# Performance work log

Measured on AMD Instinct MI355X. Metric: run time of the kernel, lower is better.

## Reference

```python
import jax, jax.numpy as jnp
import numpy as np

B, N, OUTERDIM, DIM, N_CLASSES = 2, 6000, 1024, 512, 2
HEADS, DIM_HEAD, INNER = 8, 64, 512
LANDMARKS, PINV_ITERS, KPAD = 256, 6, 16  # residual conv kernel 33 -> pad 16
SCALE = DIM_HEAD ** -0.5


def layer_norm(x, g, b, eps=1e-5):
    mu = x.mean(-1, keepdims=True)
    var = jnp.var(x, axis=-1, keepdims=True)
    return (x - mu) * jax.lax.rsqrt(var + eps) * g + b


def moore_penrose_pinv(x, iters=PINV_ITERS):
    # x: [b, h, m, m]
    abs_x = jnp.abs(x)
    col = abs_x.sum(-1)
    row = abs_x.sum(-2)
    z = jnp.swapaxes(x, -1, -2) / (jnp.max(col) * jnp.max(row))
    I = jnp.eye(x.shape[-1], dtype=x.dtype)
    for _ in range(iters):
        xz = x @ z
        z = 0.25 * z @ (13 * I - xz @ (15 * I - xz @ (7 * I - xz)))
    return z


def nystrom_attention(x, w_qkv, w_out, b_out, conv_w):
    b, n, _ = x.shape
    pad = (-n) % LANDMARKS
    xp = jnp.pad(x, ((0, 0), (pad, 0), (0, 0)))  # pad at FRONT, as in lucidrains impl
    npad = n + pad
    qkv = xp @ w_qkv.T  # [b, npad, 3*inner]
    q, k, v = [t.reshape(b, npad, HEADS, DIM_HEAD).transpose(0, 2, 1, 3)
               for t in jnp.split(qkv, 3, axis=-1)]
    q = q * SCALE
    l = npad // LANDMARKS  # tokens per landmark
    q_l = q.reshape(b, HEADS, LANDMARKS, l, DIM_HEAD).sum(3) / l
    k_l = k.reshape(b, HEADS, LANDMARKS, l, DIM_HEAD).sum(3) / l
    attn1 = jax.nn.softmax(jnp.einsum('bhid,bhjd->bhij', q, k_l), axis=-1)   # [b,h,npad,m]
    attn2 = jax.nn.softmax(jnp.einsum('bhid,bhjd->bhij', q_l, k_l), axis=-1)  # [b,h,m,m]
    attn3 = jax.nn.softmax(jnp.einsum('bhid,bhjd->bhij', q_l, k), axis=-1)    # [b,h,m,npad]
    out = (attn1 @ moore_penrose_pinv(attn2)) @ (attn3 @ v)  # [b,h,npad,d]
    # depthwise residual conv over sequence dim (per head), kernel (33,1)
    out = out + jax.lax.conv_general_dilated(
        v, conv_w, window_strides=(1, 1), padding=((KPAD, KPAD), (0, 0)),
        dimension_numbers=('NCHW', 'OIHW', 'NCHW'), feature_group_count=HEADS)
    out = out.transpose(0, 2, 1, 3).reshape(b, npad, INNER)
    out = out @ w_out.T + b_out
    return out[:, -n:]


def setup_inputs() -> dict:
    key = jax.random.key(0)
    ks = jax.random.split(key, 12)
    w = lambda k, shape: 0.02 * jax.random.normal(k, shape, dtype=jnp.float32)
    inp = {
        'data': jax.random.normal(ks[0], (B, N, OUTERDIM), dtype=jnp.float32),
        'w1': w(ks[1], (DIM, OUTERDIM)), 'b1': jnp.zeros((DIM,), jnp.float32),
        'cls_token': jax.random.normal(ks[2], (1, 1, DIM), dtype=jnp.float32),
        'ln1_g': jnp.ones((DIM,), jnp.float32), 'ln1_b': jnp.zeros((DIM,), jnp.float32),
        'qkv1_w': w(ks[3], (3 * INNER, DIM)),
        'out1_w': w(ks[4], (DIM, INNER)), 'out1_b': jnp.zeros((DIM,), jnp.float32),
        'conv1_w': w(ks[5], (HEADS, 1, 33, 1)),
        'ln2_g': jnp.ones((DIM,), jnp.float32), 'ln2_b': jnp.zeros((DIM,), jnp.float32),
        'qkv2_w': w(ks[6], (3 * INNER, DIM)),
        'out2_w': w(ks[7], (DIM, INNER)), 'out2_b': jnp.zeros((DIM,), jnp.float32),
        'conv2_w': w(ks[8], (HEADS, 1, 33, 1)),
        'lnf_g': jnp.ones((DIM,), jnp.float32), 'lnf_b': jnp.zeros((DIM,), jnp.float32),
        'w2': w(ks[9], (N_CLASSES, DIM)), 'b2': jnp.zeros((N_CLASSES,), jnp.float32),
    }
    return inp


def reference(data, w1, b1, cls_token, ln1_g, ln1_b, qkv1_w, out1_w, out1_b, conv1_w,
              ln2_g, ln2_b, qkv2_w, out2_w, out2_b, conv2_w, lnf_g, lnf_b, w2, b2):
    h = jax.nn.relu(data @ w1.T + b1)  # [B, N, DIM]
    H = h.shape[1]
    side = int(np.ceil(np.sqrt(H)))
    add = side * side - H
    h = jnp.concatenate([h, h[:, :add]], axis=1)  # square padding: 6084
    cls = jnp.broadcast_to(cls_token, (h.shape[0], 1, h.shape[2]))
    h = jnp.concatenate([cls, h], axis=1)  # +CLS: 6085
    h = h + nystrom_attention(layer_norm(h, ln1_g, ln1_b), qkv1_w, out1_w, out1_b, conv1_w)
    h = h + nystrom_attention(layer_norm(h, ln2_g, ln2_b), qkv2_w, out2_w, out2_b, conv2_w)
    h = layer_norm(h, lnf_g, lnf_b)[:, 0]
    logits = h @ w2.T + b2
    return logits
```

## Files before the change

### kernel.cpp

```cpp
#include <hip/hip_runtime.h>
#include <cstdint>
#include <cstddef>

namespace {

constexpr int DIMC  = 512;
constexpr int SEQ   = 6085;
constexpr int NPAD  = 6144;
constexpr int PADF  = 59;
constexpr int LMK   = 256;
constexpr int BHN   = 16;
constexpr int KSPL  = 16;
constexpr int MPADR = 6016;

typedef __attribute__((ext_vector_type(8))) short bf8_t;
typedef __attribute__((ext_vector_type(4))) float f4_t;

#define SWZB(r, cu) (((((r) << 6) + ((cu) << 1))) ^ (((r) & 7) << 4))

#define GLDS16(gp, lp) __builtin_amdgcn_global_load_lds( \
    (const __attribute__((address_space(1))) void*)(gp), \
    (__attribute__((address_space(3))) void*)(lp), 16, 0, 0)

__device__ __forceinline__ ushort f2bf(float f) {
    union { float f; uint32_t u; } c{f};
    uint32_t u = c.u;
    return (ushort)((u + 0x7FFFu + ((u >> 16) & 1u)) >> 16);
}
__device__ __forceinline__ float bf2f(ushort u) {
    union { uint32_t u; float f; } c{(uint32_t)u << 16};
    return c.f;
}

__device__ __forceinline__ float waveSum(float v) {
#pragma unroll
    for (int o = 32; o > 0; o >>= 1) v += __shfl_xor(v, o, 64);
    return v;
}
__device__ __forceinline__ float waveMax(float v) {
#pragma unroll
    for (int o = 32; o > 0; o >>= 1) v = fmaxf(v, __shfl_xor(v, o, 64));
    return v;
}
__device__ __forceinline__ float blockSum256(float v, float* sm) {
    v = waveSum(v);
    __syncthreads();
    if ((threadIdx.x & 63) == 0) sm[threadIdx.x >> 6] = v;
    __syncthreads();
    return sm[0] + sm[1] + sm[2] + sm[3];
}
__device__ __forceinline__ float blockMax256(float v, float* sm) {
    v = waveMax(v);
    __syncthreads();
    if ((threadIdx.x & 63) == 0) sm[threadIdx.x >> 6] = v;
    __syncthreads();
    return fmaxf(fmaxf(sm[0], sm[1]), fmaxf(sm[2], sm[3]));
}

template<int EPI>
__global__ __launch_bounds__(256)
void gemm_bt(const ushort* __restrict__ A, const ushort* __restrict__ B,
             void* __restrict__ Cv, int M, int N, int K,
             int lda, int ldb, int ldc,
             long long sA, long long sB, long long sC,
             const float* __restrict__ bias, int relu,
             ushort* __restrict__ qp, ushort* __restrict__ kp, ushort* __restrict__ vp)
{
    __shared__ __align__(16) char As_s[128 * 128];
    __shared__ __align__(16) char Bs_s[128 * 128];
    const int z = blockIdx.z;
    const ushort* Ab = A + (size_t)z * sA;
    const ushort* Bb = B + (size_t)z * sB;
    const int row0 = blockIdx.y * 128, col0 = blockIdx.x * 128;
    const int tid = threadIdx.x, wid = tid >> 6, lane = tid & 63;
    const int wr = wid >> 1, wc = wid & 1, lr = lane & 15, kg = lane >> 4;
    const int srow = lane >> 3, sq = lane & 7;
    f4_t acc[4][4] = {};
    for (int k0 = 0; k0 < K; k0 += 64) {
        __syncthreads();
#pragma unroll
        for (int i = 0; i < 4; ++i) {
            int r = wid * 32 + i * 8 + srow;
            int qs = sq ^ (r & 7);
            GLDS16(Ab + (size_t)(row0 + r) * lda + k0 + qs * 8,
                   As_s + (wid * 32 + i * 8) * 128);
        }
#pragma unroll
        for (int i = 0; i < 4; ++i) {
            int r = wid * 32 + i * 8 + srow;
            int qs = sq ^ (r & 7);
            GLDS16(Bb + (size_t)(col0 + r) * ldb + k0 + qs * 8,
                   Bs_s + (wid * 32 + i * 8) * 128);
        }
        asm volatile("s_waitcnt vmcnt(0)" ::: "memory");
        __syncthreads();
#pragma unroll
        for (int ks = 0; ks < 2; ++ks) {
            bf8_t af[4], bg[4];
#pragma unroll
            for (int mr = 0; mr < 4; ++mr) {
                int r = wr * 64 + mr * 16 + lr;
                af[mr] = *(const bf8_t*)(As_s + r * 128 + ((((ks << 2) | kg) ^ (r & 7)) << 4));
            }
#pragma unroll
            for (int nr = 0; nr < 4; ++nr) {
                int r = wc * 64 + nr * 16 + lr;
                bg[nr] = *(const bf8_t*)(Bs_s + r * 128 + ((((ks << 2) | kg) ^ (r & 7)) << 4));
            }
#pragma unroll
            for (int mr = 0; mr < 4; ++mr)
#pragma unroll
                for (int nr = 0; nr < 4; ++nr)
                    acc[mr][nr] = __builtin_amdgcn_mfma_f32_16x16x32_bf16(af[mr], bg[nr], acc[mr][nr], 0, 0, 0);
        }
    }
#pragma unroll
    for (int mr = 0; mr < 4; ++mr) {
#pragma unroll
        for (int nr = 0; nr < 4; ++nr) {
#pragma unroll
            for (int r = 0; r < 4; ++r) {
                int gm = row0 + wr * 64 + mr * 16 + kg * 4 + r;
                int gn = col0 + wc * 64 + nr * 16 + lr;
                if (gm >= M || gn >= N) continue;
                float val = acc[mr][nr][r];
                if (EPI == 0) {
                    if (bias) val += bias[gn];
                    if (relu) val = fmaxf(val, 0.f);
                    ((float*)Cv)[(size_t)z * sC + (size_t)gm * ldc + gn] = val;
                } else if (EPI == 1) {
                    ((ushort*)Cv)[(size_t)z * sC + (size_t)gm * ldc + gn] = f2bf(val);
                } else {
                    int b = (gm >= NPAD) ? 1 : 0;
                    int i = gm - b * NPAD;
                    int which = gn >> 9, hh = (gn >> 6) & 7, d = gn & 63;
                    size_t dst = ((size_t)(b * 8 + hh) * NPAD + i) * 64 + d;
                    if (which == 0)      qp[dst] = f2bf(val * 0.125f);
                    else if (which == 1) kp[dst] = f2bf(val);
                    else                 vp[dst] = f2bf(val);
                }
            }
        }
    }
}

__global__ __launch_bounds__(256)
void attn1_fused(const ushort* __restrict__ q, const ushort* __restrict__ kl,
                 const ushort* __restrict__ Wt, ushort* __restrict__ ot)
{
    __shared__ __align__(16) char P_s[128 * 512];
    const int mt = blockIdx.x;
    const int bh = blockIdx.y;
    const int b = bh >> 3, hh = bh & 7;
    const int tid = threadIdx.x, wid = tid >> 6, lane = tid & 63;
    const int lr = lane & 15, kg = lane >> 4;
    const int row0 = mt * 128;
    const ushort* qb  = q  + (size_t)bh * NPAD * 64;
    const ushort* klb = kl + (size_t)bh * LMK * 64;
    const ushort* Wtb = Wt + (size_t)bh * 128 * 256;

    f4_t acc[2][16];
#pragma unroll
    for (int mf = 0; mf < 2; ++mf)
#pragma unroll
        for (int nf = 0; nf < 16; ++nf) acc[mf][nf] = (f4_t){0.f, 0.f, 0.f, 0.f};
#pragma unroll
    for (int ks = 0; ks < 2; ++ks) {
        bf8_t af[2];
#pragma unroll
        for (int mf = 0; mf < 2; ++mf)
            af[mf] = *(const bf8_t*)&qb[(size_t)(row0 + wid * 32 + mf * 16 + lr) * 64 + ks * 32 + kg * 8];
#pragma unroll
        for (int nf = 0; nf < 16; ++nf) {
            bf8_t bg = *(const bf8_t*)&klb[(size_t)(nf * 16 + lr) * 64 + ks * 32 + kg * 8];
            acc[0][nf] = __builtin_amdgcn_mfma_f32_16x16x32_bf16(af[0], bg, acc[0][nf], 0, 0, 0);
            acc[1][nf] = __builtin_amdgcn_mfma_f32_16x16x32_bf16(af[1], bg, acc[1][nf], 0, 0, 0);
        }
    }
    float inv_s[2][4];
#pragma unroll
    for (int mf = 0; mf < 2; ++mf) {
        float mx[4] = {-1e30f, -1e30f, -1e30f, -1e30f};
#pragma unroll
        for (int nf = 0; nf < 16; ++nf)
#pragma unroll
            for (int r = 0; r < 4; ++r) mx[r] = fmaxf(mx[r], acc[mf][nf][r]);
#pragma unroll
        for (int r = 0; r < 4; ++r) {
            mx[r] = fmaxf(mx[r], __shfl_xor(mx[r], 1, 64));
            mx[r] = fmaxf(mx[r], __shfl_xor(mx[r], 2, 64));
            mx[r] = fmaxf(mx[r], __shfl_xor(mx[r], 4, 64));
            mx[r] = fmaxf(mx[r], __shfl_xor(mx[r], 8, 64));
        }
        float sum[4] = {0.f, 0.f, 0.f, 0.f};
        const int rowb = wid * 32 + mf * 16 + kg * 4;
        const int cc2 = (lr & 7) * 2;
        const int chi = lr >> 3;
#pragma unroll
        for (int nf = 0; nf < 16; ++nf) {
#pragma unroll
            for (int r = 0; r < 4; ++r) {
                float e = expf(acc[mf][nf][r] - mx[r]);
                sum[r] += e;
                int row = rowb + r;
                int chunk = (2 * nf + chi) ^ (row & 7);
                *(ushort*)(P_s + row * 512 + chunk * 16 + cc2) = f2bf(e);
            }
        }
#pragma unroll
        for (int r = 0; r < 4; ++r) {
            sum[r] += __shfl_xor(sum[r], 1, 64);
            sum[r] += __shfl_xor(sum[r], 2, 64);
            sum[r] += __shfl_xor(sum[r], 4, 64);
            sum[r] += __shfl_xor(sum[r], 8, 64);
            inv_s[mf][r] = 1.f / sum[r];
        }
    }
    f4_t acc2[2][4] = {};
#pragma unroll
    for (int kt = 0; kt < 8; ++kt) {
        bf8_t af2[2];
#pragma unroll
        for (int mf = 0; mf < 2; ++mf) {
            int row = wid * 32 + mf * 16 + lr;
            int chunk = (kt * 4 + kg) ^ (row & 7);
            af2[mf] = *(const bf8_t*)(P_s + row * 512 + chunk * 16);
        }
#pragma unroll
        for (int nf = 0; nf < 4; ++nf) {
            bf8_t bg = *(const bf8_t*)&Wtb[(size_t)(nf * 16 + lr) * 256 + kt * 32 + kg * 8];
            acc2[0][nf] = __builtin_amdgcn_mfma_f32_16x16x32_bf16(af2[0], bg, acc2[0][nf], 0, 0, 0);
            acc2[1][nf] = __builtin_amdgcn_mfma_f32_16x16x32_bf16(af2[1], bg, acc2[1][nf], 0, 0, 0);
        }
    }
#pragma unroll
    for (int mf = 0; mf < 2; ++mf)
#pragma unroll
        for (int nf = 0; nf < 4; ++nf)
#pragma unroll
            for (int r = 0; r < 4; ++r) {
                int gm = row0 + wid * 32 + mf * 16 + kg * 4 + r;
                int gn = nf * 16 + lr;
                ot[((size_t)(b * NPAD + gm)) * DIMC + hh * 64 + gn] =
                    f2bf(acc2[mf][nf][r] * inv_s[mf][r]);
            }
}

__global__ __launch_bounds__(256)
void gemm_ns(const ushort* __restrict__ A, const ushort* __restrict__ B,
             ushort* __restrict__ C, ushort* __restrict__ C2, ushort* __restrict__ CT,
             float alpha, float c2d, int K, int N,
             long long sA, long long sB, long long sC, long long sCT)
{
    __shared__ __align__(16) char As_s[64 * 64];
    __shared__ __align__(16) char Bs_s[64 * 64];
    const int z = blockIdx.z;
    const int row0 = blockIdx.y * 64, col0 = blockIdx.x * 64;
    const int tid = threadIdx.x;
    const int wid = tid >> 6, lane = tid & 63;
    const int lr = lane & 15, kg = lane >> 4;
    const ushort* Ab = A + (size_t)z * sA;
    const ushort* Bb = B + (size_t)z * sB;
    f4_t acc[4] = {};
    const int am = tid >> 2, ac8 = (tid & 3) * 8;
    for (int k0 = 0; k0 < K; k0 += 32) {
        *(bf8_t*)(As_s + SWZB(am, ac8)) = *(const bf8_t*)&Ab[(size_t)(row0 + am) * K + k0 + ac8];
#pragma unroll
        for (int p = 0; p < 8; ++p) {
            int kk = p * 4 + (tid >> 6), n = tid & 63;
            *(ushort*)(Bs_s + SWZB(n, kk)) = Bb[(size_t)(k0 + kk) * N + col0 + n];
        }
        __syncthreads();
        bf8_t af = *(const bf8_t*)(As_s + SWZB(wid * 16 + lr, kg * 8));
#pragma unroll
        for (int j = 0; j < 4; ++j) {
            bf8_t bg = *(const bf8_t*)(Bs_s + SWZB(j * 16 + lr, kg * 8));
            acc[j] = __builtin_amdgcn_mfma_f32_16x16x32_bf16(af, bg, acc[j], 0, 0, 0);
        }
        __syncthreads();
    }
#pragma unroll
    for (int j = 0; j < 4; ++j) {
#pragma unroll
        for (int r = 0; r < 4; ++r) {
            int gm = row0 + wid * 16 + kg * 4 + r;
            int gn = col0 + j * 16 + lr;
            float val = alpha * acc[j][r];
            if (C)  C[(size_t)z * sC + (size_t)gm * N + gn] = f2bf(val);
            if (C2) C2[(size_t)z * sC + (size_t)gm * N + gn] = f2bf(((gm == gn) ? c2d : 0.f) - val);
            if (CT) CT[(size_t)z * sCT + (size_t)gn * LMK + gm] = f2bf(val);
        }
    }
}

__global__ __launch_bounds__(256)
void pv_splitk(const ushort* __restrict__ S, const ushort* __restrict__ v,
               float* __restrict__ o2p)
{
    __shared__ __align__(16) char As_s[128 * 64];
    __shared__ __align__(16) char Bs_s[64 * 64];
    const int split = blockIdx.x, mt = blockIdx.y, bh = blockIdx.z;
    const int tid = threadIdx.x;
    const int wid = tid >> 6, lane = tid & 63;
    const int lr = lane & 15, kg = lane >> 4;
    const ushort* Sb = S + (size_t)bh * LMK * NPAD + (size_t)(mt * 128) * NPAD;
    const ushort* vb = v + (size_t)bh * NPAD * 64;
    const int ks0 = split * (NPAD / KSPL);
    f4_t acc[2][4] = {};
    for (int k0 = ks0; k0 < ks0 + NPAD / KSPL; k0 += 32) {
#pragma unroll
        for (int p = 0; p < 2; ++p) {
            int idx = p * 256 + tid;
            int m = idx >> 2, kc = (idx & 3) * 8;
            *(bf8_t*)(As_s + SWZB(m, kc)) = *(const bf8_t*)&Sb[(size_t)m * NPAD + k0 + kc];
        }
#pragma unroll
        for (int p = 0; p < 8; ++p) {
            int kk = p * 4 + (tid >> 6), n = tid & 63;
            *(ushort*)(Bs_s + SWZB(n, kk)) = vb[(size_t)(k0 + kk) * 64 + n];
        }
        __syncthreads();
        bf8_t af[2], bg[4];
#pragma unroll
        for (int i = 0; i < 2; ++i)
            af[i] = *(const bf8_t*)(As_s + SWZB(wid * 32 + i * 16 + lr, kg * 8));
#pragma unroll
        for (int j = 0; j < 4; ++j)
            bg[j] = *(const bf8_t*)(Bs_s + SWZB(j * 16 + lr, kg * 8));
#pragma unroll
        for (int i = 0; i < 2; ++i)
#pragma unroll
            for (int j = 0; j < 4; ++j)
                acc[i][j] = __builtin_amdgcn_mfma_f32_16x16x32_bf16(af[i], bg[j], acc[i][j], 0, 0, 0);
        __syncthreads();
    }
#pragma unroll
    for (int i = 0; i < 2; ++i)
#pragma unroll
        for (int j = 0; j < 4; ++j)
#pragma unroll
            for (int r = 0; r < 4; ++r) {
                int gm = mt * 128 + wid * 32 + i * 16 + kg * 4 + r;
                int gn = j * 16 + lr;
                o2p[((size_t)(split * BHN + bh) * LMK + gm) * 64 + gn] = acc[i][j][r];
            }
}

__global__ void reduce_o2(const float* __restrict__ o2p, ushort* __restrict__ o2) {
    int idx = blockIdx.x * 256 + threadIdx.x;
    int bh = idx >> 14, e = idx & 16383;
    float s = 0.f;
#pragma unroll
    for (int sp = 0; sp < KSPL; ++sp)
        s += o2p[((size_t)(sp * BHN + bh) << 14) + e];
    o2[idx] = f2bf(s);
}

__global__ void cvt_bf16(const float* __restrict__ in, ushort* __restrict__ out, int n8) {
    int i = blockIdx.x * 256 + threadIdx.x;
    if (i >= n8) return;
    float4 a = ((const float4*)in)[i * 2], b = ((const float4*)in)[i * 2 + 1];
    ushort4 lo = { f2bf(a.x), f2bf(a.y), f2bf(a.z), f2bf(a.w) };
    ushort4 hi = { f2bf(b.x), f2bf(b.y), f2bf(b.z), f2bf(b.w) };
    ((ushort4*)out)[i * 2] = lo;
    ((ushort4*)out)[i * 2 + 1] = hi;
}

__global__ void extend_h(float* __restrict__ h, const float* __restrict__ cls) {
    int b = blockIdx.y, bx = blockIdx.x;
    float* hb = h + (size_t)b * SEQ * DIMC;
    for (int c = threadIdx.x; c < DIMC; c += 256) {
        if (bx == 0) hb[c] = cls[c];
        else hb[(size_t)(6000 + bx) * DIMC + c] = hb[(size_t)bx * DIMC + c];
    }
}

__global__ void zero_xp_pad(ushort* __restrict__ xp) {
    int e = blockIdx.x * 256 + threadIdx.x;
    int b = e / (PADF * DIMC);
    int rest = e - b * (PADF * DIMC);
    xp[(size_t)b * NPAD * DIMC + rest] = 0;
}

__global__ __launch_bounds__(128)
void ln_to_xp(const float* __restrict__ h, const float* __restrict__ g,
              const float* __restrict__ bb, ushort* __restrict__ xp)
{
    __shared__ float sm[2];
    int r = blockIdx.x;
    int b = r / SEQ, i = r - b * SEQ;
    int t = threadIdx.x;
    const float4* row = (const float4*)(h + (size_t)r * DIMC);
    float4 x = row[t];
    float s  = x.x + x.y + x.z + x.w;
    float sq = x.x * x.x + x.y * x.y + x.z * x.z + x.w * x.w;
    s = waveSum(s);
    sq = waveSum(sq);
    int w = t >> 6;
    if ((t & 63) == 0) sm[w] = s;
    __syncthreads();
    float S = sm[0] + sm[1];
    __syncthreads();
    if ((t & 63) == 0) sm[w] = sq;
    __syncthreads();
    float SQ = sm[0] + sm[1];
    float mu = S * (1.f / DIMC);
    float var = SQ * (1.f / DIMC) - mu * mu;
    float rs = rsqrtf(var + 1e-5f);
    float4 gg = ((const float4*)g)[t];
    float4 bv = ((const float4*)bb)[t];
    ushort4 o;
    o.x = f2bf((x.x - mu) * rs * gg.x + bv.x);
    o.y = f2bf((x.y - mu) * rs * gg.y + bv.y);
    o.z = f2bf((x.z - mu) * rs * gg.z + bv.z);
    o.w = f2bf((x.w - mu) * rs * gg.w + bv.w);
    ((ushort4*)(xp + ((size_t)b * NPAD + PADF + i) * DIMC))[t] = o;
}

__global__ void landmark_mean(const ushort* __restrict__ in, ushort* __restrict__ out) {
    int m = blockIdx.x, bh = blockIdx.y, d = threadIdx.x;
    const ushort* p = in + ((size_t)bh * NPAD + (size_t)m * (NPAD / LMK)) * 64 + d;
    float s = 0.f;
#pragma unroll
    for (int j = 0; j < NPAD / LMK; ++j) s += bf2f(p[(size_t)j * 64]);
    out[((size_t)bh * LMK + m) * 64 + d] = f2bf(s * (1.f / (NPAD / LMK)));
}

__global__ __launch_bounds__(256)
void softmax_bf_wide(ushort* __restrict__ S) {
    __shared__ float sm[4];
    ushort* p = S + (size_t)blockIdx.x * NPAD;
    int t = threadIdx.x;
    float v[24];
    float mx = -1e30f;
#pragma unroll
    for (int j = 0; j < 24; ++j) { v[j] = bf2f(p[j * 256 + t]); mx = fmaxf(mx, v[j]); }
    float bm = blockMax256(mx, sm);
    float s = 0.f;
#pragma unroll
    for (int j = 0; j < 24; ++j) { v[j] = expf(v[j] - bm); s += v[j]; }
    float bs = blockSum256(s, sm);
    float inv = 1.f / bs;
#pragma unroll
    for (int j = 0; j < 24; ++j) p[j * 256 + t] = f2bf(v[j] * inv);
}

__global__ __launch_bounds__(256)
void softmax_bf256(ushort* __restrict__ S) {
    __shared__ float sm[4];
    ushort* p = S + (size_t)blockIdx.x * 256;
    int t = threadIdx.x;
    float v = bf2f(p[t]);
    float bm = blockMax256(v, sm);
    float e = expf(v - bm);
    float bs = blockSum256(e, sm);
    p[t] = f2bf(e / bs);
}

__global__ __launch_bounds__(256)
void colsum_max(const ushort* __restrict__ X, float* __restrict__ scal) {
    __shared__ float sm[4];
    int bh = blockIdx.x, t = threadIdx.x;
    const ushort* Xb = X + ((size_t)bh << 16);
    float s = 0.f;
#pragma unroll 8
    for (int i = 0; i < 256; ++i) s += bf2f(Xb[(size_t)i * 256 + t]);
    float m = blockMax256(s, sm);
    if (t == 0) atomicMax((unsigned int*)scal, __float_as_uint(m));
}

__global__ void init_z(const ushort* __restrict__ X, const float* __restrict__ scal,
                       ushort* __restrict__ Z) {
    size_t e = (size_t)blockIdx.x * 256 + threadIdx.x;
    int c = (int)(e & 255);
    int r = (int)((e >> 8) & 255);
    size_t bh = e >> 16;
    float inv = 1.f / scal[0];
    Z[e] = f2bf(bf2f(X[(bh << 16) + (size_t)c * 256 + r]) * inv);
}

__global__ __launch_bounds__(256)
void conv_add(const ushort* __restrict__ v, const float* __restrict__ cw,
              ushort* __restrict__ ot)
{
    __shared__ float w[33];
    __shared__ ushort vt[96][64];
    int bh = blockIdx.y;
    int b = bh >> 3, hh = bh & 7;
    int i0 = blockIdx.x * 64;
    int t = threadIdx.x;
    if (t < 33) w[t] = cw[hh * 33 + t];
    const ushort* vb = v + (size_t)bh * NPAD * 64;
    int d = t & 63;
    for (int rr = t >> 6; rr < 96; rr += 4) {
        int j = i0 - 16 + rr;
        vt[rr][d] = (j >= 0 && j < NPAD) ? vb[(size_t)j * 64 + d] : (ushort)0;
    }
    __syncthreads();
    for (int ii = t >> 6; ii < 64; ii += 4) {
        float acc = 0.f;
#pragma unroll
        for (int kk = 0; kk < 33; ++kk) acc += w[kk] * bf2f(vt[ii + kk][d]);
        size_t off = ((size_t)(b * NPAD + i0 + ii)) * DIMC + hh * 64 + d;
        ot[off] = f2bf(bf2f(ot[off]) + acc);
    }
}

__global__ void residual_add(float* __restrict__ h, const float* __restrict__ y) {
    size_t e = (size_t)blockIdx.x * 256 + threadIdx.x;
    int c = (int)(e & 511);
    size_t ri = e >> 9;
    int i = (int)(ri % SEQ);
    int b = (int)(ri / SEQ);
    h[e] += y[((size_t)b * NPAD + PADF + i) * DIMC + c];
}

__global__ __launch_bounds__(256)
void final_head(const float* __restrict__ h, const float* __restrict__ g,
                const float* __restrict__ bb, const float* __restrict__ w2,
                const float* __restrict__ b2, float* __restrict__ out)
{
    __shared__ float row[DIMC];
    __shared__ float sm[4];
    int b = blockIdx.x;
    int t = threadIdx.x;
    const float* x = h + (size_t)b * SEQ * DIMC;
    float v0 = x[t], v1 = x[t + 256];
    float S = blockSum256(v0 + v1, sm);
    float SQ = blockSum256(v0 * v0 + v1 * v1, sm);
    float mu = S * (1.f / DIMC);
    float rs = rsqrtf(SQ * (1.f / DIMC) - mu * mu + 1e-5f);
    row[t] = (v0 - mu) * rs * g[t] + bb[t];
    row[t + 256] = (v1 - mu) * rs * g[t + 256] + bb[t + 256];
    __syncthreads();
    if (t < 64) {
        float a0 = 0.f, a1 = 0.f;
        for (int idx = t; idx < DIMC; idx += 64) {
            a0 += row[idx] * w2[idx];
            a1 += row[idx] * w2[DIMC + idx];
        }
        a0 = waveSum(a0);
        a1 = waveSum(a1);
        if (t == 0) {
            out[b * 2 + 0] = a0 + b2[0];
            out[b * 2 + 1] = a1 + b2[1];
        }
    }
}

void bt(int epi, const ushort* A, const ushort* B, void* C, int M, int N, int K,
        int lda, int ldb, int ldc, long long sA, long long sB, long long sC, int batch,
        const float* bias, int relu, ushort* qp, ushort* kp, ushort* vp, hipStream_t s)
{
    dim3 g((N + 127) / 128, (M + 127) / 128, batch), blk(256);
    switch (epi) {
    case 0: gemm_bt<0><<<g, blk, 0, s>>>(A, B, C, M, N, K, lda, ldb, ldc, sA, sB, sC, bias, relu, qp, kp, vp); break;
    case 1: gemm_bt<1><<<g, blk, 0, s>>>(A, B, C, M, N, K, lda, ldb, ldc, sA, sB, sC, bias, relu, qp, kp, vp); break;
    default: gemm_bt<2><<<g, blk, 0, s>>>(A, B, C, M, N, K, lda, ldb, ldc, sA, sB, sC, bias, relu, qp, kp, vp); break;
    }
}

void ns(const ushort* A, const ushort* B, ushort* C, ushort* C2, ushort* CT,
        float alpha, float c2d, int M, int N, int K,
        long long sA, long long sB, long long sC, long long sCT, hipStream_t s)
{
    dim3 g(N / 64, M / 64, BHN), blk(256);
    gemm_ns<<<g, blk, 0, s>>>(A, B, C, C2, CT, alpha, c2d, K, N, sA, sB, sC, sCT);
}

struct WS {
    float *h, *scal, *o2p, *y;
    ushort *xp, *q, *k, *v, *ql, *kl;
    ushort *datab, *w1b, *qkvwb1, *qkvwb2, *outwb1, *outwb2;
    ushort *X, *Z0, *Z1, *XZ, *TA, *TB, *TC;
    ushort *o2b, *Wt, *S, *ot;
};

void nystrom_layer(float* h, const float* lng, const float* lnb,
                   const ushort* qkvwb, const ushort* outwb, const float* outb,
                   const float* convw, const WS& w, hipStream_t s)
{
    const long long SM = (long long)LMK * LMK;
    zero_xp_pad<<<(2 * PADF * DIMC) / 256, 256, 0, s>>>(w.xp);
    ln_to_xp<<<2 * SEQ, 128, 0, s>>>(h, lng, lnb, w.xp);
    bt(2, w.xp, qkvwb, nullptr, 2 * NPAD, 3 * DIMC, DIMC, DIMC, DIMC, 0,
       0, 0, 0, 1, nullptr, 0, w.q, w.k, w.v, s);
    landmark_mean<<<dim3(LMK, BHN), 64, 0, s>>>(w.q, w.ql);
    landmark_mean<<<dim3(LMK, BHN), 64, 0, s>>>(w.k, w.kl);
    bt(1, w.ql, w.kl, w.X, LMK, LMK, 64, 64, 64, LMK,
       (long long)LMK * 64, (long long)LMK * 64, SM, BHN, nullptr, 0, nullptr, nullptr, nullptr, s);
    softmax_bf256<<<BHN * LMK, 256, 0, s>>>(w.X);
    hipMemsetAsync(w.scal, 0, 8, s);
    colsum_max<<<BHN, 256, 0, s>>>(w.X, w.scal);
    init_z<<<(BHN * LMK * LMK) / 256, 256, 0, s>>>(w.X, w.scal, w.Z0);
    ushort* Zc = w.Z0;
    ushort* Zn = w.Z1;
    for (int it = 0; it < 6; ++it) {
        ns(w.X, Zc, w.XZ, w.TA, nullptr, 1.f, 7.f, LMK, LMK, LMK, SM, SM, SM, 0, s);
        ns(w.XZ, w.TA, w.TB, w.TC, nullptr, 1.f, 15.f, LMK, LMK, LMK, SM, SM, SM, 0, s);
        ns(w.XZ, w.TC, w.TB, w.TA, nullptr, 1.f, 13.f, LMK, LMK, LMK, SM, SM, SM, 0, s);
        ns(Zc, w.TA, Zn, nullptr, nullptr, 0.25f, 0.f, LMK, LMK, LMK, SM, SM, SM, 0, s);
        ushort* t = Zc; Zc = Zn; Zn = t;
    }
    bt(1, w.ql, w.k, w.S, LMK, NPAD, 64, 64, 64, NPAD,
       (long long)LMK * 64, (long long)NPAD * 64, (long long)LMK * NPAD, BHN,
       nullptr, 0, nullptr, nullptr, nullptr, s);
    softmax_bf_wide<<<BHN * LMK, 256, 0, s>>>(w.S);
    pv_splitk<<<dim3(KSPL, 2, BHN), 256, 0, s>>>(w.S, w.v, w.o2p);
    reduce_o2<<<BHN * LMK * 64 / 256, 256, 0, s>>>(w.o2p, w.o2b);
    ns(Zc, w.o2b, nullptr, nullptr, w.Wt, 1.f, 0.f, LMK, 64, LMK,
       SM, (long long)LMK * 64, 0, 128 * 256, s);
    attn1_fused<<<dim3(NPAD / 128, BHN), 256, 0, s>>>(w.q, w.kl, w.Wt, w.ot);
    conv_add<<<dim3(NPAD / 64, BHN), 256, 0, s>>>(w.v, convw, w.ot);
    bt(0, w.ot, outwb, w.y, 2 * NPAD, DIMC, DIMC, DIMC, DIMC, DIMC,
       0, 0, 0, 1, outb, 0, nullptr, nullptr, nullptr, s);
    residual_add<<<(2 * SEQ * DIMC) / 256, 256, 0, s>>>(h, w.y);
}

}

extern "C" void kernel_launch(void* const* d_in, const int* in_sizes, int n_in,
                              void* d_out, int out_size, void* d_ws, size_t ws_size,
                              hipStream_t stream)
{
    (void)in_sizes; (void)n_in; (void)out_size;
    const float* data  = (const float*)d_in[0];
    const float* w1    = (const float*)d_in[1];
    const float* b1    = (const float*)d_in[2];
    const float* cls   = (const float*)d_in[3];
    const float* ln1g  = (const float*)d_in[4];
    const float* ln1b  = (const float*)d_in[5];
    const float* qkv1w = (const float*)d_in[6];
    const float* out1w = (const float*)d_in[7];
    const float* out1b = (const float*)d_in[8];
    const float* conv1 = (const float*)d_in[9];
    const float* ln2g  = (const float*)d_in[10];
    const float* ln2b  = (const float*)d_in[11];
    const float* qkv2w = (const float*)d_in[12];
    const float* out2w = (const float*)d_in[13];
    const float* out2b = (const float*)d_in[14];
    const float* conv2 = (const float*)d_in[15];
    const float* lnfg  = (const float*)d_in[16];
    const float* lnfb  = (const float*)d_in[17];
    const float* w2    = (const float*)d_in[18];
    const float* b2    = (const float*)d_in[19];
    float* out = (float*)d_out;

    if (ws_size < 209473792ull) return;
    char* p = (char*)d_ws;
    auto alloc = [&](size_t bytes) { char* r = p; p += (bytes + 255) & ~(size_t)255; return r; };
    WS w;
    w.h     = (float*)alloc((size_t)2 * SEQ * DIMC * 4);
    w.xp    = (ushort*)alloc((size_t)2 * NPAD * DIMC * 2);
    w.q     = (ushort*)alloc((size_t)BHN * NPAD * 64 * 2);
    w.k     = (ushort*)alloc((size_t)BHN * NPAD * 64 * 2);
    w.v     = (ushort*)alloc((size_t)BHN * NPAD * 64 * 2);
    w.ql    = (ushort*)alloc((size_t)BHN * LMK * 64 * 2);
    w.kl    = (ushort*)alloc((size_t)BHN * LMK * 64 * 2);
    w.scal  = (float*)alloc(256);
    w.datab = (ushort*)alloc((size_t)2 * MPADR * 1024 * 2);
    w.w1b   = (ushort*)alloc((size_t)512 * 1024 * 2);
    w.qkvwb1= (ushort*)alloc((size_t)1536 * 512 * 2);
    w.qkvwb2= (ushort*)alloc((size_t)1536 * 512 * 2);
    w.outwb1= (ushort*)alloc((size_t)512 * 512 * 2);
    w.outwb2= (ushort*)alloc((size_t)512 * 512 * 2);
    w.X     = (ushort*)alloc((size_t)BHN * LMK * LMK * 2);
    w.Z0    = (ushort*)alloc((size_t)BHN * LMK * LMK * 2);
    w.Z1    = (ushort*)alloc((size_t)BHN * LMK * LMK * 2);
    w.XZ    = (ushort*)alloc((size_t)BHN * LMK * LMK * 2);
    w.TA    = (ushort*)alloc((size_t)BHN * LMK * LMK * 2);
    w.TB    = (ushort*)alloc((size_t)BHN * LMK * LMK * 2);
    w.TC    = (ushort*)alloc((size_t)BHN * LMK * LMK * 2);
    w.o2p   = (float*)alloc((size_t)KSPL * BHN * LMK * 64 * 4);
    w.o2b   = (ushort*)alloc((size_t)BHN * LMK * 64 * 2);
    w.Wt    = (ushort*)alloc((size_t)BHN * 128 * 256 * 2);
    w.S     = (ushort*)alloc((size_t)BHN * LMK * NPAD * 2);
    w.y     = (float*)w.S;
    w.ot    = w.k;

    for (int b = 0; b < 2; ++b)
        cvt_bf16<<<3000, 256, 0, stream>>>(data + (size_t)b * 6000 * 1024,
                                           w.datab + (size_t)b * MPADR * 1024, 768000);
    cvt_bf16<<<256, 256, 0, stream>>>(w1, w.w1b, 65536);
    cvt_bf16<<<384, 256, 0, stream>>>(qkv1w, w.qkvwb1, 98304);
    cvt_bf16<<<384, 256, 0, stream>>>(qkv2w, w.qkvwb2, 98304);
    cvt_bf16<<<128, 256, 0, stream>>>(out1w, w.outwb1, 32768);
    cvt_bf16<<<128, 256, 0, stream>>>(out2w, w.outwb2, 32768);

    bt(0, w.datab, w.w1b, w.h + DIMC, 6000, DIMC, 1024, 1024, 1024, DIMC,
       (long long)MPADR * 1024, 0, (long long)SEQ * DIMC, 2, b1, 1,
       nullptr, nullptr, nullptr, stream);
    extend_h<<<dim3(85, 2), 256, 0, stream>>>(w.h, cls);

    nystrom_layer(w.h, ln1g, ln1b, w.qkvwb1, w.outwb1, out1b, conv1, w, stream);
    nystrom_layer(w.h, ln2g, ln2b, w.qkvwb2, w.outwb2, out2b, conv2, w, stream);

    final_head<<<2, 256, 0, stream>>>(w.h, lnfg, lnfb, w2, b2, out);
}
```

Before: 1.019 ms.

## Remap GEMM blocks across XCDs, halve attn1 tile rows, use fast exp

Block indices in the generic GEMM are remapped so that consecutive tiles land on the same XCD, which should improve L2 reuse on the multi-die part. attn1_fused now handles 64 rows per block with one 16-row fragment per wave, halving the accumulator registers and shared memory to raise occupancy and double the grid. Softmax kernels switch expf to __expf, trading a little accuracy for cheaper exponentials.

```diff
diff --git a/kernel.cpp b/kernel.cpp
--- a/kernel.cpp
+++ b/kernel.cpp
@@ -16,6 +16,8 @@
 typedef __attribute__((ext_vector_type(8))) short bf8_t;
 typedef __attribute__((ext_vector_type(4))) float f4_t;
 
+#define MFMA(a, b, c) __builtin_amdgcn_mfma_f32_16x16x32_bf16(a, b, c, 0, 0, 0)
+
 #define SWZB(r, cu) (((((r) << 6) + ((cu) << 1))) ^ (((r) & 7) << 4))
 
 #define GLDS16(gp, lp) __builtin_amdgcn_global_load_lds( \
@@ -55,6 +57,20 @@
     if ((threadIdx.x & 63) == 0) sm[threadIdx.x >> 6] = v;
     __syncthreads();
     return fmaxf(fmaxf(sm[0], sm[1]), fmaxf(sm[2], sm[3]));
+}
+__device__ __forceinline__ float grpMax(float v) {
+    v = fmaxf(v, __shfl_xor(v, 1, 64));
+    v = fmaxf(v, __shfl_xor(v, 2, 64));
+    v = fmaxf(v, __shfl_xor(v, 4, 64));
+    v = fmaxf(v, __shfl_xor(v, 8, 64));
+    return v;
+}
+__device__ __forceinline__ float grpSum(float v) {
+    v += __shfl_xor(v, 1, 64);
+    v += __shfl_xor(v, 2, 64);
+    v += __shfl_xor(v, 4, 64);
+    v += __shfl_xor(v, 8, 64);
+    return v;
 }
 
 template<int EPI>
@@ -68,10 +84,21 @@
 {
     __shared__ __align__(16) char As_s[128 * 128];
     __shared__ __align__(16) char Bs_s[128 * 128];
-    const int z = blockIdx.z;
+    const int gx = gridDim.x, gy = gridDim.y;
+    const int total = gx * gy * gridDim.z;
+    int flat = (blockIdx.z * gy + blockIdx.y) * gx + blockIdx.x;
+    {
+        int q = total >> 3, r = total & 7;
+        int xcd = flat & 7, idx = flat >> 3;
+        flat = (xcd < r ? xcd * (q + 1) : r * (q + 1) + (xcd - r) * q) + idx;
+    }
+    const int z = flat / (gx * gy);
+    const int rem = flat - z * gx * gy;
+    const int by = rem / gx, bx = rem - by * gx;
+
     const ushort* Ab = A + (size_t)z * sA;
     const ushort* Bb = B + (size_t)z * sB;
-    const int row0 = blockIdx.y * 128, col0 = blockIdx.x * 128;
+    const int row0 = by * 128, col0 = bx * 128;
     const int tid = threadIdx.x, wid = tid >> 6, lane = tid & 63;
     const int wr = wid >> 1, wc = wid & 1, lr = lane & 15, kg = lane >> 4;
     const int srow = lane >> 3, sq = lane & 7;
@@ -111,7 +138,7 @@
             for (int mr = 0; mr < 4; ++mr)
 #pragma unroll
                 for (int nr = 0; nr < 4; ++nr)
-                    acc[mr][nr] = __builtin_amdgcn_mfma_f32_16x16x32_bf16(af[mr], bg[nr], acc[mr][nr], 0, 0, 0);
+                    acc[mr][nr] = MFMA(af[mr], bg[nr], acc[mr][nr]);
         }
     }
 #pragma unroll
@@ -134,116 +161,17 @@
                     int b = (gm >= NPAD) ? 1 : 0;
                     int i = gm - b * NPAD;
                     int which = gn >> 9, hh = (gn >> 6) & 7, d = gn & 63;
-                    size_t dst = ((size_t)(b * 8 + hh) * NPAD + i) * 64 + d;
-                    if (which == 0)      qp[dst] = f2bf(val * 0.125f);
-                    else if (which == 1) kp[dst] = f2bf(val);
-                    else                 vp[dst] = f2bf(val);
+                    int bh = b * 8 + hh;
+                    if (which == 0)
+                        qp[((size_t)bh * NPAD + i) * 64 + d] = f2bf(val * 0.125f);
+                    else if (which == 1)
+                        kp[((size_t)bh * NPAD + i) * 64 + d] = f2bf(val);
+                    else
+                        vp[((size_t)bh * NPAD + i) * 64 + d] = f2bf(val);
                 }
             }
         }
     }
-}
-
-__global__ __launch_bounds__(256)
-void attn1_fused(const ushort* __restrict__ q, const ushort* __restrict__ kl,
-                 const ushort* __restrict__ Wt, ushort* __restrict__ ot)
-{
-    __shared__ __align__(16) char P_s[128 * 512];
-    const int mt = blockIdx.x;
-    const int bh = blockIdx.y;
-    const int b = bh >> 3, hh = bh & 7;
-    const int tid = threadIdx.x, wid = tid >> 6, lane = tid & 63;
-    const int lr = lane & 15, kg = lane >> 4;
-    const int row0 = mt * 128;
-    const ushort* qb  = q  + (size_t)bh * NPAD * 64;
-    const ushort* klb = kl + (size_t)bh * LMK * 64;
-    const ushort* Wtb = Wt + (size_t)bh * 128 * 256;
-
-    f4_t acc[2][16];
-#pragma unroll
-    for (int mf = 0; mf < 2; ++mf)
-#pragma unroll
-        for (int nf = 0; nf < 16; ++nf) acc[mf][nf] = (f4_t){0.f, 0.f, 0.f, 0.f};
-#pragma unroll
-    for (int ks = 0; ks < 2; ++ks) {
-        bf8_t af[2];
-#pragma unroll
-        for (int mf = 0; mf < 2; ++mf)
-            af[mf] = *(const bf8_t*)&qb[(size_t)(row0 + wid * 32 + mf * 16 + lr) * 64 + ks * 32 + kg * 8];
-#pragma unroll
-        for (int nf = 0; nf < 16; ++nf) {
-            bf8_t bg = *(const bf8_t*)&klb[(size_t)(nf * 16 + lr) * 64 + ks * 32 + kg * 8];
-            acc[0][nf] = __builtin_amdgcn_mfma_f32_16x16x32_bf16(af[0], bg, acc[0][nf], 0, 0, 0);
-            acc[1][nf] = __builtin_amdgcn_mfma_f32_16x16x32_bf16(af[1], bg, acc[1][nf], 0, 0, 0);
-        }
-    }
-    float inv_s[2][4];
-#pragma unroll
-    for (int mf = 0; mf < 2; ++mf) {
-        float mx[4] = {-1e30f, -1e30f, -1e30f, -1e30f};
-#pragma unroll
-        for (int nf = 0; nf < 16; ++nf)
-#pragma unroll
-            for (int r = 0; r < 4; ++r) mx[r] = fmaxf(mx[r], acc[mf][nf][r]);
-#pragma unroll
-        for (int r = 0; r < 4; ++r) {
-            mx[r] = fmaxf(mx[r], __shfl_xor(mx[r], 1, 64));
-            mx[r] = fmaxf(mx[r], __shfl_xor(mx[r], 2, 64));
-            mx[r] = fmaxf(mx[r], __shfl_xor(mx[r], 4, 64));
-            mx[r] = fmaxf(mx[r], __shfl_xor(mx[r], 8, 64));
-        }
-        float sum[4] = {0.f, 0.f, 0.f, 0.f};
-        const int rowb = wid * 32 + mf * 16 + kg * 4;
-        const int cc2 = (lr & 7) * 2;
-        const int chi = lr >> 3;
-#pragma unroll
-        for (int nf = 0; nf < 16; ++nf) {
-#pragma unroll
-            for (int r = 0; r < 4; ++r) {
-                float e = expf(acc[mf][nf][r] - mx[r]);
-                sum[r] += e;
-                int row = rowb + r;
-                int chunk = (2 * nf + chi) ^ (row & 7);
-                *(ushort*)(P_s + row * 512 + chunk * 16 + cc2) = f2bf(e);
-            }
-        }
-#pragma unroll
-        for (int r = 0; r < 4; ++r) {
-            sum[r] += __shfl_xor(sum[r], 1, 64);
-            sum[r] += __shfl_xor(sum[r], 2, 64);
-            sum[r] += __shfl_xor(sum[r], 4, 64);
-            sum[r] += __shfl_xor(sum[r], 8, 64);
-            inv_s[mf][r] = 1.f / sum[r];
-        }
-    }
-    f4_t acc2[2][4] = {};
-#pragma unroll
-    for (int kt = 0; kt < 8; ++kt) {
-        bf8_t af2[2];
-#pragma unroll
-        for (int mf = 0; mf < 2; ++mf) {
-            int row = wid * 32 + mf * 16 + lr;
-            int chunk = (kt * 4 + kg) ^ (row & 7);
-            af2[mf] = *(const bf8_t*)(P_s + row * 512 + chunk * 16);
-        }
-#pragma unroll
-        for (int nf = 0; nf < 4; ++nf) {
-            bf8_t bg = *(const bf8_t*)&Wtb[(size_t)(nf * 16 + lr) * 256 + kt * 32 + kg * 8];
-            acc2[0][nf] = __builtin_amdgcn_mfma_f32_16x16x32_bf16(af2[0], bg, acc2[0][nf], 0, 0, 0);
-            acc2[1][nf] = __builtin_amdgcn_mfma_f32_16x16x32_bf16(af2[1], bg, acc2[1][nf], 0, 0, 0);
-        }
-    }
-#pragma unroll
-    for (int mf = 0; mf < 2; ++mf)
-#pragma unroll
-        for (int nf = 0; nf < 4; ++nf)
-#pragma unroll
-            for (int r = 0; r < 4; ++r) {
-                int gm = row0 + wid * 32 + mf * 16 + kg * 4 + r;
-                int gn = nf * 16 + lr;
-                ot[((size_t)(b * NPAD + gm)) * DIMC + hh * 64 + gn] =
-                    f2bf(acc2[mf][nf][r] * inv_s[mf][r]);
-            }
 }
 
 __global__ __launch_bounds__(256)
@@ -275,7 +203,7 @@
 #pragma unroll
         for (int j = 0; j < 4; ++j) {
             bf8_t bg = *(const bf8_t*)(Bs_s + SWZB(j * 16 + lr, kg * 8));
-            acc[j] = __builtin_amdgcn_mfma_f32_16x16x32_bf16(af, bg, acc[j], 0, 0, 0);
+            acc[j] = MFMA(af, bg, acc[j]);
         }
         __syncthreads();
     }
@@ -331,7 +259,7 @@
         for (int i = 0; i < 2; ++i)
 #pragma unroll
             for (int j = 0; j < 4; ++j)
-                acc[i][j] = __builtin_amdgcn_mfma_f32_16x16x32_bf16(af[i], bg[j], acc[i][j], 0, 0, 0);
+                acc[i][j] = MFMA(af[i], bg[j], acc[i][j]);
         __syncthreads();
     }
 #pragma unroll
@@ -354,6 +282,80 @@
     for (int sp = 0; sp < KSPL; ++sp)
         s += o2p[((size_t)(sp * BHN + bh) << 14) + e];
     o2[idx] = f2bf(s);
+}
+
+__global__ __launch_bounds__(256)
+void attn1_fused(const ushort* __restrict__ q, const ushort* __restrict__ kl,
+                 const ushort* __restrict__ Wt, ushort* __restrict__ ot)
+{
+    __shared__ __align__(16) char P_s[64 * 512];
+    const int mt = blockIdx.x;
+    const int bh = blockIdx.y;
+    const int b = bh >> 3, hh = bh & 7;
+    const int tid = threadIdx.x, wid = tid >> 6, lane = tid & 63;
+    const int lr = lane & 15, kg = lane >> 4;
+    const int row0 = mt * 64, rowb = wid * 16;
+    const ushort* qb  = q  + (size_t)bh * NPAD * 64;
+    const ushort* klb = kl + (size_t)bh * LMK * 64;
+    const ushort* Wtb = Wt + (size_t)bh * 128 * 256;
+
+    f4_t acc[16];
+#pragma unroll
+    for (int nf = 0; nf < 16; ++nf) acc[nf] = (f4_t){0.f, 0.f, 0.f, 0.f};
+#pragma unroll
+    for (int ks = 0; ks < 2; ++ks) {
+        bf8_t af = *(const bf8_t*)&qb[(size_t)(row0 + rowb + lr) * 64 + ks * 32 + kg * 8];
+#pragma unroll
+        for (int nf = 0; nf < 16; ++nf) {
+            bf8_t bg = *(const bf8_t*)&klb[(size_t)(nf * 16 + lr) * 64 + ks * 32 + kg * 8];
+            acc[nf] = MFMA(af, bg, acc[nf]);
+        }
+    }
+    float inv_s[4];
+    {
+        float mx[4] = {-3.0e38f, -3.0e38f, -3.0e38f, -3.0e38f};
+#pragma unroll
+        for (int nf = 0; nf < 16; ++nf)
+#pragma unroll
+            for (int r = 0; r < 4; ++r) mx[r] = fmaxf(mx[r], acc[nf][r]);
+#pragma unroll
+        for (int r = 0; r < 4; ++r) mx[r] = grpMax(mx[r]);
+        float sum[4] = {0.f, 0.f, 0.f, 0.f};
+        const int rb2 = rowb + kg * 4;
+        const int cc2 = (lr & 7) * 2, chi = lr >> 3;
+#pragma unroll
+        for (int nf = 0; nf < 16; ++nf)
+#pragma unroll
+            for (int r = 0; r < 4; ++r) {
+                float e = __expf(acc[nf][r] - mx[r]);
+                sum[r] += e;
+                int row = rb2 + r;
+                int chunk = (2 * nf + chi) ^ (row & 7);
+                *(ushort*)(P_s + row * 512 + chunk * 16 + cc2) = f2bf(e);
+            }
+#pragma unroll
+        for (int r = 0; r < 4; ++r) inv_s[r] = 1.f / grpSum(sum[r]);
+    }
+    f4_t acc2[4] = {};
+#pragma unroll
+    for (int kt = 0; kt < 8; ++kt) {
+        int row = rowb + lr;
+        int chunk = (kt * 4 + kg) ^ (row & 7);
+        bf8_t af2 = *(const bf8_t*)(P_s + row * 512 + chunk * 16);
+#pragma unroll
+        for (int nf = 0; nf < 4; ++nf) {
+            bf8_t bg = *(const bf8_t*)&Wtb[(size_t)(nf * 16 + lr) * 256 + kt * 32 + kg * 8];
+            acc2[nf] = MFMA(af2, bg, acc2[nf]);
+        }
+    }
+#pragma unroll
+    for (int nf = 0; nf < 4; ++nf)
+#pragma unroll
+        for (int r = 0; r < 4; ++r) {
+            int gm = row0 + rowb + kg * 4 + r;
+            int gn = nf * 16 + lr;
+            ot[((size_t)(b * NPAD + gm)) * DIMC + hh * 64 + gn] = f2bf(acc2[nf][r] * inv_s[r]);
+        }
 }
 
 __global__ void cvt_bf16(const float* __restrict__ in, ushort* __restrict__ out, int n8) {
@@ -438,7 +440,7 @@
     float bm = blockMax256(mx, sm);
     float s = 0.f;
 #pragma unroll
-    for (int j = 0; j < 24; ++j) { v[j] = expf(v[j] - bm); s += v[j]; }
+    for (int j = 0; j < 24; ++j) { v[j] = __expf(v[j] - bm); s += v[j]; }
     float bs = blockSum256(s, sm);
     float inv = 1.f / bs;
 #pragma unroll
@@ -452,7 +454,7 @@
     int t = threadIdx.x;
     float v = bf2f(p[t]);
     float bm = blockMax256(v, sm);
-    float e = expf(v - bm);
+    float e = __expf(v - bm);
     float bs = blockSum256(e, sm);
     p[t] = f2bf(e / bs);
 }
@@ -588,7 +590,8 @@
     landmark_mean<<<dim3(LMK, BHN), 64, 0, s>>>(w.q, w.ql);
     landmark_mean<<<dim3(LMK, BHN), 64, 0, s>>>(w.k, w.kl);
     bt(1, w.ql, w.kl, w.X, LMK, LMK, 64, 64, 64, LMK,
-       (long long)LMK * 64, (long long)LMK * 64, SM, BHN, nullptr, 0, nullptr, nullptr, nullptr, s);
+       (long long)LMK * 64, (long long)LMK * 64, SM, BHN,
+       nullptr, 0, nullptr, nullptr, nullptr, s);
     softmax_bf256<<<BHN * LMK, 256, 0, s>>>(w.X);
     hipMemsetAsync(w.scal, 0, 8, s);
     colsum_max<<<BHN, 256, 0, s>>>(w.X, w.scal);
@@ -610,7 +613,7 @@
     reduce_o2<<<BHN * LMK * 64 / 256, 256, 0, s>>>(w.o2p, w.o2b);
     ns(Zc, w.o2b, nullptr, nullptr, w.Wt, 1.f, 0.f, LMK, 64, LMK,
        SM, (long long)LMK * 64, 0, 128 * 256, s);
-    attn1_fused<<<dim3(NPAD / 128, BHN), 256, 0, s>>>(w.q, w.kl, w.Wt, w.ot);
+    attn1_fused<<<dim3(NPAD / 64, BHN), 256, 0, s>>>(w.q, w.kl, w.Wt, w.ot);
     conv_add<<<dim3(NPAD / 64, BHN), 256, 0, s>>>(w.v, convw, w.ot);
     bt(0, w.ot, outwb, w.y, 2 * NPAD, DIMC, DIMC, DIMC, DIMC, DIMC,
        0, 0, 0, 1, outb, 0, nullptr, nullptr, nullptr, s);
```

Result: no change. 1.017 ms (-0.2%).
